# Performance work log

Measured on AMD Instinct MI355X. Metric: run time of the kernel, lower is better.

Reference implementation:

```python
import jax, jax.numpy as jnp
import numpy as np


def setup_inputs() -> dict:
    key = jax.random.key(0)
    k1, k2, k3, k4 = jax.random.split(key, 4)
    B, S, D = 2, 2048, 1024
    return {
        "X": jax.random.normal(k1, (B, S, D), dtype=jnp.float32),
        "W_q": jax.random.normal(k2, (D, D), dtype=jnp.float32),
        "W_k": jax.random.normal(k3, (D, D), dtype=jnp.float32),
        "W_v": jax.random.normal(k4, (D, D), dtype=jnp.float32),
        "n_heads": 16,
    }


def reference(X, W_q, W_k, W_v, n_heads):
    B, S, D = X.shape
    H = n_heads
    dh = D // H
    # QKV projections, split heads: [B,S,D] -> [H,B,S,dh]
    def split_heads(Y):
        return Y.reshape(B, S, H, dh).transpose(2, 0, 1, 3)
    Q = split_heads(X @ W_q)
    K = split_heads(X @ W_k)
    V = split_heads(X @ W_v)
    scale = 1.0 / jnp.sqrt(jnp.asarray(dh, dtype=X.dtype))
    # [H,B,S,S] attention scores (naive, matches the original)
    scores = jax.nn.softmax(jnp.einsum("hbqd,hbkd->hbqk", Q, K) * scale, axis=-1)
    out = jnp.einsum("hbqk,hbkd->hbqd", scores, V)  # [H,B,S,dh]
    # torch.concat(out, 0) over leading H dim -> [H*B, S, dh]
    return out.reshape(H * B, S, dh)
```

## Files before the change

kernel.cpp:

```cpp
#include <hip/hip_runtime.h>

typedef unsigned short u16;
typedef unsigned int u32;
typedef __bf16 bf16x8 __attribute__((ext_vector_type(8)));
typedef float f32x4 __attribute__((ext_vector_type(4)));
typedef float f32x16 __attribute__((ext_vector_type(16)));

extern "C" __device__ float __ocml_native_exp2_f32(float);

#define WT_HI_E  ((size_t)0)
#define WT_LO_E  ((size_t)3 << 20)
#define X_HI_E   ((size_t)6 << 20)
#define X_LO_E   ((size_t)10 << 20)
#define Q_HI_E   ((size_t)14 << 20)
#define Q_LO_E   ((size_t)18 << 20)
#define K_HI_E   ((size_t)22 << 20)
#define K_LO_E   ((size_t)26 << 20)
#define V_HI_E   ((size_t)30 << 20)
#define O1_E     ((size_t)0)
#define ML_E     ((size_t)9 << 20)

__device__ __forceinline__ u16 bf16_rne(float x) {
  u32 u = __float_as_uint(x);
  u32 r = (u + 0x7fffu + ((u >> 16) & 1u)) >> 16;
  return (u16)r;
}
__device__ __forceinline__ float bf16_f(u16 h) {
  return __uint_as_float(((u32)h) << 16);
}

__device__ __forceinline__ void gload16(const u16* g, u16* l) {
  __builtin_amdgcn_global_load_lds(
      (const __attribute__((address_space(1))) void*)g,
      (__attribute__((address_space(3))) void*)l, 16, 0, 0);
}

__global__ __launch_bounds__(256) void k_split(const float* __restrict__ X,
                                               const float* __restrict__ w0,
                                               const float* __restrict__ w1,
                                               const float* __restrict__ w2,
                                               u16* __restrict__ ws) {
  int bid = blockIdx.x;
  if (bid < 2048) {
    u16* xh = ws + X_HI_E;
    u16* xl = ws + X_LO_E;
    size_t i = ((size_t)bid * 256 + threadIdx.x) * 8;
    float4 a = *(const float4*)(X + i);
    float4 b = *(const float4*)(X + i + 4);
    float v[8] = {a.x, a.y, a.z, a.w, b.x, b.y, b.z, b.w};
    u32 Hh[4], Ll[4];
#pragma unroll
    for (int j = 0; j < 4; j++) {
      u16 h0 = bf16_rne(v[2 * j]);
      u16 l0 = bf16_rne(v[2 * j] - bf16_f(h0));
      u16 h1 = bf16_rne(v[2 * j + 1]);
      u16 l1 = bf16_rne(v[2 * j + 1] - bf16_f(h1));
      Hh[j] = (u32)h0 | ((u32)h1 << 16);
      Ll[j] = (u32)l0 | ((u32)l1 << 16);
    }
    *(uint4*)(xh + i) = make_uint4(Hh[0], Hh[1], Hh[2], Hh[3]);
    *(uint4*)(xl + i) = make_uint4(Ll[0], Ll[1], Ll[2], Ll[3]);
  } else {
    int wb = bid - 2048;
    int z = wb >> 10;
    int rem = wb & 1023;
    int by = (rem >> 5) * 32, bx = (rem & 31) * 32;
    const float* W = (z == 0) ? w0 : ((z == 1) ? w1 : w2);
    u16* th = ws + WT_HI_E + (size_t)z * (1u << 20);
    u16* tl = ws + WT_LO_E + (size_t)z * (1u << 20);
    __shared__ float tile[32][33];
    int tx = threadIdx.x & 31, ty = threadIdx.x >> 5;
#pragma unroll
    for (int i = 0; i < 4; i++) {
      int r = ty + i * 8;
      tile[r][tx] = W[(size_t)(by + r) * 1024 + bx + tx];
    }
    __syncthreads();
#pragma unroll
    for (int i = 0; i < 4; i++) {
      int r = ty + i * 8;
      float v = tile[tx][r];
      int n = bx + r, k = by + tx;
      u16 h = bf16_rne(v);
      u16 l = bf16_rne(v - bf16_f(h));
      th[(size_t)n * 1024 + k] = h;
      tl[(size_t)n * 1024 + k] = l;
    }
  }
}

__global__ __launch_bounds__(256, 4) void k_proj(u16* __restrict__ ws) {
  int id = blockIdx.x;
  int xcd = id & 7;
  int loc = id >> 3;
  int m_loc = loc & 7;
  int rest = loc >> 3;
  int n_blk = rest & 7, z = rest >> 3;
  int M0 = (xcd * 8 + m_loc) * 64;
  int N0 = n_blk * 128;

  const u16* Xh = ws + X_HI_E;
  const u16* Xl = ws + X_LO_E;
  const u16* Wh = ws + WT_HI_E + (size_t)z * (1u << 20);
  const u16* Wl = ws + WT_LO_E + (size_t)z * (1u << 20);
  u16* dsth = ws + ((z == 0) ? Q_HI_E : ((z == 1) ? K_HI_E : V_HI_E));
  u16* dstl = (z == 0) ? (ws + Q_LO_E) : ((z == 1) ? (ws + K_LO_E) : (u16*)0);

  __shared__ u16 sXh[2048], sXl[2048], sWh[4096], sWl[4096];
  int tid = threadIdx.x, lane = tid & 63, w = tid >> 6;
  int quad = lane >> 4, l16 = lane & 15;
  int mb = (w & 1) * 32, nb = (w >> 1) * 64;

  const f32x4 z4 = {0.f, 0.f, 0.f, 0.f};
  f32x4 acc[2][4];
#pragma unroll
  for (int i = 0; i < 2; i++)
#pragma unroll
    for (int j = 0; j < 4; j++) acc[i][j] = z4;

  int xrow = tid >> 2, xq8 = tid & 3;

  for (int kk = 0; kk < 1024; kk += 32) {
    __syncthreads();
    {
      size_t gx = (size_t)(M0 + xrow) * 1024 + kk + xq8 * 8;
      gload16(Xh + gx, &sXh[(size_t)(w * 16) * 32]);
      if (z != 2) gload16(Xl + gx, &sXl[(size_t)(w * 16) * 32]);
#pragma unroll
      for (int j = 0; j < 2; j++) {
        int c = tid + 256 * j;
        int row = c >> 2, q8 = c & 3;
        size_t gw = (size_t)(N0 + row) * 1024 + kk + q8 * 8;
        gload16(Wh + gw, &sWh[(size_t)(j * 64 + w * 16) * 32]);
        if (z != 2) gload16(Wl + gw, &sWl[(size_t)(j * 64 + w * 16) * 32]);
      }
    }
    __syncthreads();
    bf16x8 ah[2], bh[4];
#pragma unroll
    for (int i = 0; i < 2; i++)
      ah[i] = *(const bf16x8*)&sXh[(mb + i * 16 + l16) * 32 + quad * 8];
#pragma unroll
    for (int j = 0; j < 4; j++)
      bh[j] = *(const bf16x8*)&sWh[(nb + j * 16 + l16) * 32 + quad * 8];
    if (z != 2) {
      bf16x8 al[2], bl[4];
#pragma unroll
      for (int i = 0; i < 2; i++)
        al[i] = *(const bf16x8*)&sXl[(mb + i * 16 + l16) * 32 + quad * 8];
#pragma unroll
      for (int j = 0; j < 4; j++)
        bl[j] = *(const bf16x8*)&sWl[(nb + j * 16 + l16) * 32 + quad * 8];
#pragma unroll
      for (int i = 0; i < 2; i++)
#pragma unroll
        for (int j = 0; j < 4; j++) {
          f32x4 c0 = acc[i][j];
          c0 = __builtin_amdgcn_mfma_f32_16x16x32_bf16(ah[i], bh[j], c0, 0, 0, 0);
          c0 = __builtin_amdgcn_mfma_f32_16x16x32_bf16(ah[i], bl[j], c0, 0, 0, 0);
          c0 = __builtin_amdgcn_mfma_f32_16x16x32_bf16(al[i], bh[j], c0, 0, 0, 0);
          acc[i][j] = c0;
        }
    } else {
#pragma unroll
      for (int i = 0; i < 2; i++)
#pragma unroll
        for (int j = 0; j < 4; j++)
          acc[i][j] = __builtin_amdgcn_mfma_f32_16x16x32_bf16(ah[i], bh[j], acc[i][j], 0, 0, 0);
    }
  }

  if (z == 2) {
#pragma unroll
    for (int i = 0; i < 2; i++)
#pragma unroll
      for (int j = 0; j < 4; j++) {
        int mg = M0 + mb + i * 16 + quad * 4;
        int ng = N0 + nb + j * 16 + l16;
        int b = mg >> 11, s = mg & 2047;
        int hh = ng >> 6, d = ng & 63;
        u16 p0 = bf16_rne(acc[i][j][0]);
        u16 p1 = bf16_rne(acc[i][j][1]);
        u16 p2 = bf16_rne(acc[i][j][2]);
        u16 p3 = bf16_rne(acc[i][j][3]);
        *(uint2*)&dsth[((size_t)(hh * 2 + b) * 64 + d) * 2048 + s] =
            make_uint2((u32)p0 | ((u32)p1 << 16), (u32)p2 | ((u32)p3 << 16));
      }
  } else {
    float qscale = (z == 0) ? (0.125f * 1.4426950408889634f) : 1.0f;
#pragma unroll
    for (int i = 0; i < 2; i++)
#pragma unroll
      for (int j = 0; j < 4; j++)
#pragma unroll
        for (int r = 0; r < 4; r++) {
          int mg = M0 + mb + i * 16 + quad * 4 + r;
          int ng = N0 + nb + j * 16 + l16;
          int b = mg >> 11, s = mg & 2047;
          int hh = ng >> 6, d = ng & 63;
          size_t idx = ((size_t)(hh * 2 + b) * 2048 + s) * 64 + d;
          float y = acc[i][j][r] * qscale;
          u16 h = bf16_rne(y);
          dsth[idx] = h;
          dstl[idx] = bf16_rne(y - bf16_f(h));
        }
  }
}

__global__ __launch_bounds__(256, 4) void k_attn(u16* __restrict__ ws,
                                                 float* __restrict__ out) {
  const u16* Qh = ws + Q_HI_E;
  const u16* Ql = ws + Q_LO_E;
  const u16* Kh = ws + K_HI_E;
  const u16* Kl = ws + K_LO_E;
  const u16* Vt = ws + V_HI_E;
  float* o1 = (float*)(ws + O1_E);
  float* ml = (float*)(ws + ML_E);

  __shared__ u16 sKh[2][2048], sKl[2][2048], sVt[2][2048];

  int id = blockIdx.x;
  int hb = id & 31;
  int qb = (id >> 5) & 15, split = id >> 9;
  int kt0 = split * 1024;

  int tid = threadIdx.x, w = tid >> 6, lane = tid & 63;
  int l31 = lane & 31, h = lane >> 5;
  size_t base = (size_t)hb * (2048 * 64);
  int qw0 = qb * 128 + w * 32;

  auto stage = [&](int buf, int kt) {
    size_t kg = base + (size_t)(kt + l31) * 64 + (w * 2 + h) * 8;
    gload16(Kh + kg, &sKh[buf][w * 512]);
    gload16(Kl + kg, &sKl[buf][w * 512]);
    size_t vg = base + (size_t)lane * 2048 + kt + w * 8;
    gload16(Vt + vg, &sVt[buf][w * 512]);
  };

  stage(0, kt0);

  bf16x8 qh[4], ql[4];
#pragma unroll
  for (int ks = 0; ks < 4; ks++) {
    size_t off = base + (size_t)(qw0 + l31) * 64 + ks * 16 + h * 8;
    qh[ks] = *(const bf16x8*)(Qh + off);
    ql[ks] = *(const bf16x8*)(Ql + off);
  }

  f32x16 o[2];
#pragma unroll
  for (int i = 0; i < 16; i++) { o[0][i] = 0.f; o[1][i] = 0.f; }
  float mr = -1e30f, lr = 0.f;

  for (int it = 0; it < 32; it++) {
    __syncthreads();
    if (it + 1 < 32) stage((it + 1) & 1, kt0 + (it + 1) * 32);
    int buf = it & 1;

    f32x16 sc;
#pragma unroll
    for (int i = 0; i < 16; i++) sc[i] = 0.f;
#pragma unroll
    for (int ks = 0; ks < 4; ks++) {
      bf16x8 kh = *(const bf16x8*)&sKh[buf][((ks * 2 + h) * 32 + l31) * 8];
      bf16x8 kl = *(const bf16x8*)&sKl[buf][((ks * 2 + h) * 32 + l31) * 8];
      sc = __builtin_amdgcn_mfma_f32_32x32x16_bf16(kh, qh[ks], sc, 0, 0, 0);
      sc = __builtin_amdgcn_mfma_f32_32x32x16_bf16(kh, ql[ks], sc, 0, 0, 0);
      sc = __builtin_amdgcn_mfma_f32_32x32x16_bf16(kl, qh[ks], sc, 0, 0, 0);
    }

    float mx = sc[0];
#pragma unroll
    for (int i = 1; i < 16; i++) mx = fmaxf(mx, sc[i]);
    mx = fmaxf(mx, __shfl_xor(mx, 32));
    bool anyup = __any(mx > mr);
    float alpha = 1.f;
    if (anyup) {
      float mnew = fmaxf(mr, mx);
      alpha = __ocml_native_exp2_f32(mr - mnew);
      mr = mnew;
    }
    float rs = 0.f;
    u32 pk[8];
#pragma unroll
    for (int i = 0; i < 8; i++) {
      float p0 = __ocml_native_exp2_f32(sc[2 * i] - mr);
      float p1 = __ocml_native_exp2_f32(sc[2 * i + 1] - mr);
      rs += p0 + p1;
      u32 a = __float_as_uint(p0) + 0x8000u;
      u32 b = __float_as_uint(p1) + 0x8000u;
      pk[i] = __builtin_amdgcn_perm(b, a, 0x07060302u);
    }
    rs += __shfl_xor(rs, 32);
    lr = lr * alpha + rs;
    if (anyup) {
#pragma unroll
      for (int i = 0; i < 16; i++) {
        o[0][i] *= alpha;
        o[1][i] *= alpha;
      }
    }

#pragma unroll
    for (int ks = 0; ks < 2; ks++) {
      u32 b0 = pk[ks * 4 + 0], b1 = pk[ks * 4 + 1];
      u32 b2 = pk[ks * 4 + 2], b3 = pk[ks * 4 + 3];
      u32 rA = (u32)__shfl_xor((int)(h ? b0 : b2), 32);
      u32 rB = (u32)__shfl_xor((int)(h ? b1 : b3), 32);
      uint4 fb = h ? make_uint4(rA, rB, b2, b3) : make_uint4(b0, b1, rA, rB);
      bf16x8 pfrag = *(bf16x8*)&fb;
#pragma unroll
      for (int mt = 0; mt < 2; mt++) {
        bf16x8 vb = *(const bf16x8*)&sVt[buf][((ks * 2 + h) * 64 + mt * 32 + l31) * 8];
        o[mt] = __builtin_amdgcn_mfma_f32_32x32x16_bf16(vb, pfrag, o[mt], 0, 0, 0);
      }
    }
  }

  float* op = split ? o1 : out;
  float* mlp = ml + (size_t)split * 131072;
  size_t g = (size_t)hb * 2048 + qw0 + l31;
  if (h == 0) {
    mlp[g] = mr;
    mlp[65536 + g] = lr;
  }
#pragma unroll
  for (int mt = 0; mt < 2; mt++)
#pragma unroll
    for (int g2 = 0; g2 < 4; g2++) {
      int d0 = mt * 32 + g2 * 8 + 4 * h;
      float4 v = make_float4(o[mt][g2 * 4 + 0], o[mt][g2 * 4 + 1],
                             o[mt][g2 * 4 + 2], o[mt][g2 * 4 + 3]);
      *(float4*)(op + g * 64 + d0) = v;
    }
}

__global__ __launch_bounds__(256) void k_combine(const u16* __restrict__ ws,
                                                 float* __restrict__ out) {
  const float* o1 = (const float*)(ws + O1_E);
  const float* ml = (const float*)(ws + ML_E);
  size_t idx = (size_t)blockIdx.x * 256 + threadIdx.x;
  size_t g = idx >> 4;
  float m0 = ml[g], l0 = ml[65536 + g];
  float m1 = ml[131072 + g], l1 = ml[196608 + g];
  float M = fmaxf(m0, m1);
  float w0 = __ocml_native_exp2_f32(m0 - M), w1 = __ocml_native_exp2_f32(m1 - M);
  float inv = 1.f / (l0 * w0 + l1 * w1);
  float4 a = ((const float4*)out)[idx];
  float4 b = ((const float4*)o1)[idx];
  float4 r;
  r.x = (a.x * w0 + b.x * w1) * inv;
  r.y = (a.y * w0 + b.y * w1) * inv;
  r.z = (a.z * w0 + b.z * w1) * inv;
  r.w = (a.w * w0 + b.w * w1) * inv;
  ((float4*)out)[idx] = r;
}

extern "C" void kernel_launch(void* const* d_in, const int* in_sizes, int n_in,
                              void* d_out, int out_size, void* d_ws, size_t ws_size,
                              hipStream_t stream) {
  const float* X = (const float*)d_in[0];
  const float* Wq = (const float*)d_in[1];
  const float* Wk = (const float*)d_in[2];
  const float* Wv = (const float*)d_in[3];
  u16* ws = (u16*)d_ws;
  float* out = (float*)d_out;

  k_split<<<dim3(5120), dim3(256), 0, stream>>>(X, Wq, Wk, Wv, ws);
  k_proj<<<dim3(1536), dim3(256), 0, stream>>>(ws);
  k_attn<<<dim3(1024), dim3(256), 0, stream>>>(ws, out);
  k_combine<<<dim3(4096), dim3(256), 0, stream>>>(ws, out);
}
```

Measured before the change: 245.1 us.

## Pre-swizzle K/V into MFMA fragment order and load directly to registers

The projection kernel now writes K and V^T in a tiled layout that matches the MFMA operand fragment order, so the attention kernel can load K and V straight from global memory into registers with contiguous 16-byte loads. This removes the LDS double-buffering and per-iteration __syncthreads. K for the next tile is prefetched into registers while the current tile is processed. The conditional rescale (__any check) is replaced by an unconditional alpha rescale, and launch bounds drop to 3 blocks per CU to allow more registers. The trade-off is that every wave now re-reads K/V from global memory or L2 instead of sharing a staged LDS copy, and occupancy is lower.

```diff
diff --git a/kernel.cpp b/kernel.cpp
--- a/kernel.cpp
+++ b/kernel.cpp
@@ -179,11 +179,14 @@
         int ng = N0 + nb + j * 16 + l16;
         int b = mg >> 11, s = mg & 2047;
         int hh = ng >> 6, d = ng & 63;
+        size_t idx = (size_t)(hh * 2 + b) * 131072 +
+                     (size_t)(((s >> 5) * 4 + (d >> 5) * 2 + ((s >> 4) & 1)) * 64 +
+                              ((s >> 3) & 1) * 32 + (d & 31)) * 8 + (s & 7);
         u16 p0 = bf16_rne(acc[i][j][0]);
         u16 p1 = bf16_rne(acc[i][j][1]);
         u16 p2 = bf16_rne(acc[i][j][2]);
         u16 p3 = bf16_rne(acc[i][j][3]);
-        *(uint2*)&dsth[((size_t)(hh * 2 + b) * 64 + d) * 2048 + s] =
+        *(uint2*)&dsth[idx] =
             make_uint2((u32)p0 | ((u32)p1 << 16), (u32)p2 | ((u32)p3 << 16));
       }
   } else {
@@ -198,7 +201,14 @@
           int ng = N0 + nb + j * 16 + l16;
           int b = mg >> 11, s = mg & 2047;
           int hh = ng >> 6, d = ng & 63;
-          size_t idx = ((size_t)(hh * 2 + b) * 2048 + s) * 64 + d;
+          size_t idx;
+          if (z == 1) {
+            idx = (size_t)(hh * 2 + b) * 131072 +
+                  (size_t)(((s >> 5) * 4 + (d >> 4)) * 64 +
+                           ((d >> 3) & 1) * 32 + (s & 31)) * 8 + (d & 7);
+          } else {
+            idx = ((size_t)(hh * 2 + b) * 2048 + s) * 64 + d;
+          }
           float y = acc[i][j][r] * qscale;
           u16 h = bf16_rne(y);
           dsth[idx] = h;
@@ -207,7 +217,7 @@
   }
 }
 
-__global__ __launch_bounds__(256, 4) void k_attn(u16* __restrict__ ws,
+__global__ __launch_bounds__(256, 3) void k_attn(u16* __restrict__ ws,
                                                  float* __restrict__ out) {
   const u16* Qh = ws + Q_HI_E;
   const u16* Ql = ws + Q_LO_E;
@@ -217,27 +227,15 @@
   float* o1 = (float*)(ws + O1_E);
   float* ml = (float*)(ws + ML_E);
 
-  __shared__ u16 sKh[2][2048], sKl[2][2048], sVt[2][2048];
-
   int id = blockIdx.x;
   int hb = id & 31;
   int qb = (id >> 5) & 15, split = id >> 9;
-  int kt0 = split * 1024;
+  int kb0 = split * 32;
 
   int tid = threadIdx.x, w = tid >> 6, lane = tid & 63;
   int l31 = lane & 31, h = lane >> 5;
-  size_t base = (size_t)hb * (2048 * 64);
+  size_t base = (size_t)hb * 131072;
   int qw0 = qb * 128 + w * 32;
-
-  auto stage = [&](int buf, int kt) {
-    size_t kg = base + (size_t)(kt + l31) * 64 + (w * 2 + h) * 8;
-    gload16(Kh + kg, &sKh[buf][w * 512]);
-    gload16(Kl + kg, &sKl[buf][w * 512]);
-    size_t vg = base + (size_t)lane * 2048 + kt + w * 8;
-    gload16(Vt + vg, &sVt[buf][w * 512]);
-  };
-
-  stage(0, kt0);
 
   bf16x8 qh[4], ql[4];
 #pragma unroll
@@ -252,34 +250,52 @@
   for (int i = 0; i < 16; i++) { o[0][i] = 0.f; o[1][i] = 0.f; }
   float mr = -1e30f, lr = 0.f;
 
+  bf16x8 kh[4], kl[4];
+  {
+    size_t ka = base + (size_t)kb0 * 2048 + lane * 8;
+#pragma unroll
+    for (int ks = 0; ks < 4; ks++) {
+      kh[ks] = *(const bf16x8*)(Kh + ka + ks * 512);
+      kl[ks] = *(const bf16x8*)(Kl + ka + ks * 512);
+    }
+  }
+
   for (int it = 0; it < 32; it++) {
-    __syncthreads();
-    if (it + 1 < 32) stage((it + 1) & 1, kt0 + (it + 1) * 32);
-    int buf = it & 1;
-
     f32x16 sc;
 #pragma unroll
     for (int i = 0; i < 16; i++) sc[i] = 0.f;
 #pragma unroll
     for (int ks = 0; ks < 4; ks++) {
-      bf16x8 kh = *(const bf16x8*)&sKh[buf][((ks * 2 + h) * 32 + l31) * 8];
-      bf16x8 kl = *(const bf16x8*)&sKl[buf][((ks * 2 + h) * 32 + l31) * 8];
-      sc = __builtin_amdgcn_mfma_f32_32x32x16_bf16(kh, qh[ks], sc, 0, 0, 0);
-      sc = __builtin_amdgcn_mfma_f32_32x32x16_bf16(kh, ql[ks], sc, 0, 0, 0);
-      sc = __builtin_amdgcn_mfma_f32_32x32x16_bf16(kl, qh[ks], sc, 0, 0, 0);
+      sc = __builtin_amdgcn_mfma_f32_32x32x16_bf16(kh[ks], qh[ks], sc, 0, 0, 0);
+      sc = __builtin_amdgcn_mfma_f32_32x32x16_bf16(kh[ks], ql[ks], sc, 0, 0, 0);
+      sc = __builtin_amdgcn_mfma_f32_32x32x16_bf16(kl[ks], qh[ks], sc, 0, 0, 0);
+    }
+
+    bf16x8 vb[2][2];
+    {
+      size_t va = base + (size_t)(kb0 + it) * 2048 + lane * 8;
+#pragma unroll
+      for (int mt = 0; mt < 2; mt++)
+#pragma unroll
+        for (int ks = 0; ks < 2; ks++)
+          vb[mt][ks] = *(const bf16x8*)(Vt + va + (mt * 2 + ks) * 512);
+    }
+    if (it + 1 < 32) {
+      size_t ka = base + (size_t)(kb0 + it + 1) * 2048 + lane * 8;
+#pragma unroll
+      for (int ks = 0; ks < 4; ks++) {
+        kh[ks] = *(const bf16x8*)(Kh + ka + ks * 512);
+        kl[ks] = *(const bf16x8*)(Kl + ka + ks * 512);
+      }
     }
 
     float mx = sc[0];
 #pragma unroll
     for (int i = 1; i < 16; i++) mx = fmaxf(mx, sc[i]);
     mx = fmaxf(mx, __shfl_xor(mx, 32));
-    bool anyup = __any(mx > mr);
-    float alpha = 1.f;
-    if (anyup) {
-      float mnew = fmaxf(mr, mx);
-      alpha = __ocml_native_exp2_f32(mr - mnew);
-      mr = mnew;
-    }
+    float mnew = fmaxf(mr, mx);
+    float alpha = __ocml_native_exp2_f32(mr - mnew);
+    mr = mnew;
     float rs = 0.f;
     u32 pk[8];
 #pragma unroll
@@ -293,12 +309,10 @@
     }
     rs += __shfl_xor(rs, 32);
     lr = lr * alpha + rs;
-    if (anyup) {
-#pragma unroll
-      for (int i = 0; i < 16; i++) {
-        o[0][i] *= alpha;
-        o[1][i] *= alpha;
-      }
+#pragma unroll
+    for (int i = 0; i < 16; i++) {
+      o[0][i] *= alpha;
+      o[1][i] *= alpha;
     }
 
 #pragma unroll
@@ -310,10 +324,8 @@
       uint4 fb = h ? make_uint4(rA, rB, b2, b3) : make_uint4(b0, b1, rA, rB);
       bf16x8 pfrag = *(bf16x8*)&fb;
 #pragma unroll
-      for (int mt = 0; mt < 2; mt++) {
-        bf16x8 vb = *(const bf16x8*)&sVt[buf][((ks * 2 + h) * 64 + mt * 32 + l31) * 8];
-        o[mt] = __builtin_amdgcn_mfma_f32_32x32x16_bf16(vb, pfrag, o[mt], 0, 0, 0);
-      }
+      for (int mt = 0; mt < 2; mt++)
+        o[mt] = __builtin_amdgcn_mfma_f32_32x32x16_bf16(vb[mt][ks], pfrag, o[mt], 0, 0, 0);
     }
   }
 
```

New measurement: 246.7 us. No clear change (+0.7%).
